# Kernel tuning notes

Measured on AMD Instinct MI355X. Metric: run time of the kernel, lower is better.

## Reference

```python
import jax, jax.numpy as jnp
import numpy as np

DIM = 512
NUM_HEADS = 16
HEAD_DIM = DIM // NUM_HEADS
HIDDEN = int(DIM * 4.0)
EPS = 1e-5


def layer_norm(x, gamma, beta):
    mu = jnp.mean(x, axis=-1, keepdims=True)
    var = jnp.mean(jnp.square(x - mu), axis=-1, keepdims=True)
    return (x - mu) * jax.lax.rsqrt(var + EPS) * gamma + beta


def setup_inputs() -> dict:
    key = jax.random.key(0)
    ks = jax.random.split(key, 8)
    B, L, C = 32, 3136, DIM
    x = jax.random.normal(ks[0], (B, L, C), dtype=jnp.float32)
    norm1_g = jnp.ones((C,), jnp.float32)
    norm1_b = jnp.zeros((C,), jnp.float32)
    # spatial (per-head) mixing weight: (num_heads, head_dim, head_dim)
    w_spatial = jax.random.normal(ks[1], (NUM_HEADS, HEAD_DIM, HEAD_DIM), jnp.float32) * (1.0 / np.sqrt(HEAD_DIM))
    norm2_g = jnp.ones((C,), jnp.float32)
    norm2_b = jnp.zeros((C,), jnp.float32)
    w1 = jax.random.normal(ks[2], (C, HIDDEN), jnp.float32) * (1.0 / np.sqrt(C))
    b1 = jnp.zeros((HIDDEN,), jnp.float32)
    w2 = jax.random.normal(ks[3], (HIDDEN, C), jnp.float32) * (1.0 / np.sqrt(HIDDEN))
    b2 = jnp.zeros((C,), jnp.float32)
    return {"x": x, "norm1_g": norm1_g, "norm1_b": norm1_b, "w_spatial": w_spatial,
            "norm2_g": norm2_g, "norm2_b": norm2_b, "w1": w1, "b1": b1, "w2": w2, "b2": b2}


def reference(x, norm1_g, norm1_b, w_spatial, norm2_g, norm2_b, w1, b1, w2, b2):
    B, L, C = x.shape
    shortcut = x
    h = layer_norm(x, norm1_g, norm1_b)
    # window partition -> per-head channel-sub-dim linear (shared across windows/positions)
    # mathematically equivalent to applying the per-head matmul at every token
    h = h.reshape(B, L, NUM_HEADS, HEAD_DIM)
    h = jnp.einsum('blhd,hde->blhe', h, w_spatial)
    h = h.reshape(B, L, C)
    x = shortcut + h
    # channel MLP: Linear -> GELU(tanh) -> Linear
    y = layer_norm(x, norm2_g, norm2_b)
    y = jax.nn.gelu(y @ w1 + b1, approximate=True)
    y = y @ w2 + b2
    return x + y
```

## Files before the change

### kernel.cpp

```cpp
#include <hip/hip_runtime.h>
#include <hip/hip_bf16.h>


typedef __bf16 bf16x8 __attribute__((ext_vector_type(8)));
typedef float f32x4 __attribute__((ext_vector_type(4)));

constexpr int CDIM = 512;
constexpr int HID = 2048;
constexpr int MROWS = 32 * 3136;
constexpr float LN_EPS = 1e-5f;

static __device__ __forceinline__ float gelu_tanh(float x) {
  const float u = 0.7978845608028654f * fmaf(0.044715f * x * x, x, x);
  const float e = __expf(2.0f * u);
  return 0.5f * x * (2.0f - 2.0f / (e + 1.0f));
}

static __device__ __forceinline__ void load_lds16(const void* g, void* l) {
  __builtin_amdgcn_global_load_lds((__attribute__((address_space(1))) void*)g,
                                   (__attribute__((address_space(3))) void*)l,
                                   16, 0, 0);
}

template <int KD>
__global__ __launch_bounds__(256) void cvt_t(const float* __restrict__ src,
                                             __hip_bfloat16* __restrict__ dst,
                                             int ND) {
  const int i = blockIdx.x * 256 + threadIdx.x;
  const int n = i / KD;
  const int k = i - n * KD;
  dst[i] = __float2bfloat16(src[(size_t)k * ND + n]);
}

__global__ __launch_bounds__(256) void fused_pre(
    const float* __restrict__ x, const float* __restrict__ g1,
    const float* __restrict__ b1, const float* __restrict__ wsp,
    const float* __restrict__ g2, const float* __restrict__ b2,
    float* __restrict__ x2out, __hip_bfloat16* __restrict__ yout) {
  __shared__ float lnbuf[CDIM];
  __shared__ float red[8];

  const int t = threadIdx.x;
  const int lane = t & 63;
  const int w = t >> 6;
  const int c0 = t, c1 = t + 256;
  const int hd0 = c0 >> 5, e0 = c0 & 31;
  const int hd1 = c1 >> 5, e1 = c1 & 31;

  float wc0[32], wc1[32];
#pragma unroll
  for (int d = 0; d < 32; ++d) {
    wc0[d] = wsp[(hd0 * 32 + d) * 32 + e0];
    wc1[d] = wsp[(hd1 * 32 + d) * 32 + e1];
  }
  const float g1v0 = g1[c0], g1v1 = g1[c1], b1v0 = b1[c0], b1v1 = b1[c1];
  const float g2v0 = g2[c0], g2v1 = g2[c1], b2v0 = b2[c0], b2v1 = b2[c1];

  for (int r = blockIdx.x; r < MROWS; r += gridDim.x) {
    const float* xr = x + (size_t)r * CDIM;
    const float xv0 = xr[c0], xv1 = xr[c1];

    float s = xv0 + xv1, ss = xv0 * xv0 + xv1 * xv1;
#pragma unroll
    for (int off = 32; off; off >>= 1) {
      s += __shfl_down(s, off);
      ss += __shfl_down(ss, off);
    }
    if (lane == 0) { red[w * 2] = s; red[w * 2 + 1] = ss; }
    __syncthreads();
    s = red[0] + red[2] + red[4] + red[6];
    ss = red[1] + red[3] + red[5] + red[7];
    float mu = s * (1.0f / CDIM);
    float var = ss * (1.0f / CDIM) - mu * mu;
    float rs = rsqrtf(var + LN_EPS);
    lnbuf[c0] = (xv0 - mu) * rs * g1v0 + b1v0;
    lnbuf[c1] = (xv1 - mu) * rs * g1v1 + b1v1;
    __syncthreads();

    float h0 = 0.f, h1 = 0.f;
#pragma unroll
    for (int d = 0; d < 32; ++d) {
      h0 = fmaf(lnbuf[hd0 * 32 + d], wc0[d], h0);
      h1 = fmaf(lnbuf[hd1 * 32 + d], wc1[d], h1);
    }
    const float a0 = xv0 + h0, a1 = xv1 + h1;
    x2out[(size_t)r * CDIM + c0] = a0;
    x2out[(size_t)r * CDIM + c1] = a1;

    s = a0 + a1;
    ss = a0 * a0 + a1 * a1;
#pragma unroll
    for (int off = 32; off; off >>= 1) {
      s += __shfl_down(s, off);
      ss += __shfl_down(ss, off);
    }
    if (lane == 0) { red[w * 2] = s; red[w * 2 + 1] = ss; }
    __syncthreads();
    s = red[0] + red[2] + red[4] + red[6];
    ss = red[1] + red[3] + red[5] + red[7];
    mu = s * (1.0f / CDIM);
    var = ss * (1.0f / CDIM) - mu * mu;
    rs = rsqrtf(var + LN_EPS);
    yout[(size_t)r * CDIM + c0] = __float2bfloat16((a0 - mu) * rs * g2v0 + b2v0);
    yout[(size_t)r * CDIM + c1] = __float2bfloat16((a1 - mu) * rs * g2v1 + b2v1);
    __syncthreads();
  }
}

template <int K, int N, bool GELU>
__global__ __launch_bounds__(512, 2) void gemm8p(
    const __hip_bfloat16* __restrict__ A, const __hip_bfloat16* __restrict__ Bt,
    const float* __restrict__ bias, __hip_bfloat16* __restrict__ zout,
    float* __restrict__ fout) {
  constexpr int NT = N / 256;
  constexpr int NKT = K / 32;
  __shared__ __attribute__((aligned(16))) __hip_bfloat16 lds[4][2][256 * 32];

  const int tid = threadIdx.x;
  const int lane = tid & 63;
  const int w = tid >> 6;
  const int wm = w >> 2, wn = w & 3;

  const int cpx = gridDim.x >> 3;
  const int bid = (blockIdx.x & 7) * cpx + (blockIdx.x >> 3);
  const int tm = bid / NT, tn = bid - tm * NT;
  const size_t am0 = (size_t)tm * 256;
  const int bn0 = tn * 256;

  const int r0 = tid >> 2;
  const int ks0 = (tid & 3) ^ ((tid >> 2) & 3) ^ ((tid >> 4) & 3);
  const __hip_bfloat16* aP0 = A + (am0 + r0) * K + ks0 * 8;
  const __hip_bfloat16* aP1 = aP0 + (size_t)128 * K;
  const __hip_bfloat16* bP0 = Bt + (size_t)(bn0 + r0) * K + ks0 * 8;
  const __hip_bfloat16* bP1 = bP0 + (size_t)128 * K;
  const int lo0 = (w * 64) * 8;
  const int lo1 = (512 + w * 64) * 8;

#define STAGE_A(sl, kt)                            \
  do {                                             \
    load_lds16(aP0 + (kt) * 32, &lds[sl][0][lo0]); \
    load_lds16(aP1 + (kt) * 32, &lds[sl][0][lo1]); \
  } while (0)
#define STAGE_B(sl, kt)                            \
  do {                                             \
    load_lds16(bP0 + (kt) * 32, &lds[sl][1][lo0]); \
    load_lds16(bP1 + (kt) * 32, &lds[sl][1][lo1]); \
  } while (0)

  f32x4 acc[8][4] = {};
  const int fr = lane & 15;
  const int kgs = (((lane >> 4) ^ (lane & 3) ^ ((lane >> 2) & 3))) * 8;

  STAGE_A(0, 0);
  STAGE_B(0, 0);
  STAGE_A(1, 1);
  STAGE_B(1, 1);

  for (int t = 0; t < NKT; ++t) {
    if (t + 1 < NKT)
      asm volatile("s_waitcnt vmcnt(4)" ::: "memory");
    else
      asm volatile("s_waitcnt vmcnt(0)" ::: "memory");
    __builtin_amdgcn_s_barrier();

    const int sl = t & 3;
    const int s2 = (t + 2) & 3;
    const bool pf = (t + 2) < NKT;
    const __hip_bfloat16* As = lds[sl][0];
    const __hip_bfloat16* Bs = lds[sl][1];

    if (pf) STAGE_A(s2, t + 2);
    bf16x8 bfv[4];
#pragma unroll
    for (int n = 0; n < 4; ++n)
      bfv[n] = *(const bf16x8*)(Bs + (wn * 64 + n * 16 + fr) * 32 + kgs);
    bf16x8 af[4];
#pragma unroll
    for (int m = 0; m < 4; ++m)
      af[m] = *(const bf16x8*)(As + (wm * 128 + m * 16 + fr) * 32 + kgs);
    __builtin_amdgcn_s_setprio(1);
#pragma unroll
    for (int m = 0; m < 4; ++m)
#pragma unroll
      for (int n = 0; n < 4; ++n)
        acc[m][n] = __builtin_amdgcn_mfma_f32_16x16x32_bf16(af[m], bfv[n],
                                                            acc[m][n], 0, 0, 0);
    __builtin_amdgcn_s_setprio(0);
    __builtin_amdgcn_s_barrier();

    if (pf) STAGE_B(s2, t + 2);
#pragma unroll
    for (int m = 0; m < 4; ++m)
      af[m] = *(const bf16x8*)(As + (wm * 128 + (m + 4) * 16 + fr) * 32 + kgs);
    __builtin_amdgcn_s_setprio(1);
#pragma unroll
    for (int m = 0; m < 4; ++m)
#pragma unroll
      for (int n = 0; n < 4; ++n)
        acc[m + 4][n] = __builtin_amdgcn_mfma_f32_16x16x32_bf16(
            af[m], bfv[n], acc[m + 4][n], 0, 0, 0);
    __builtin_amdgcn_s_setprio(0);
  }
#undef STAGE_A
#undef STAGE_B

  const int cr = (lane >> 4) * 4;
  const int cc = lane & 15;
#pragma unroll
  for (int n = 0; n < 4; ++n) {
    const int col = bn0 + wn * 64 + n * 16 + cc;
    const float bv = bias[col];
#pragma unroll
    for (int m = 0; m < 8; ++m) {
      const size_t row = am0 + wm * 128 + m * 16 + cr;
#pragma unroll
      for (int j = 0; j < 4; ++j) {
        const float v = acc[m][n][j] + bv;
        const size_t off = (row + j) * N + col;
        if constexpr (GELU) {
          zout[off] = __float2bfloat16(gelu_tanh(v));
        } else {
          fout[off] = fout[off] + v;
        }
      }
    }
  }
}

extern "C" void kernel_launch(void* const* d_in, const int* in_sizes, int n_in,
                              void* d_out, int out_size, void* d_ws,
                              size_t ws_size, hipStream_t stream) {
  const float* x = (const float*)d_in[0];
  const float* n1g = (const float*)d_in[1];
  const float* n1b = (const float*)d_in[2];
  const float* wsp = (const float*)d_in[3];
  const float* n2g = (const float*)d_in[4];
  const float* n2b = (const float*)d_in[5];
  const float* w1 = (const float*)d_in[6];
  const float* b1 = (const float*)d_in[7];
  const float* w2 = (const float*)d_in[8];
  const float* b2 = (const float*)d_in[9];
  float* out = (float*)d_out;

  __hip_bfloat16* ybuf = (__hip_bfloat16*)d_ws;
  __hip_bfloat16* zbuf = ybuf + (size_t)MROWS * CDIM;
  __hip_bfloat16* w1t = zbuf + (size_t)MROWS * HID;
  __hip_bfloat16* w2t = w1t + (size_t)CDIM * HID;

  cvt_t<CDIM><<<(CDIM * HID) / 256, 256, 0, stream>>>(w1, w1t, HID);
  cvt_t<HID><<<(CDIM * HID) / 256, 256, 0, stream>>>(w2, w2t, CDIM);
  fused_pre<<<2048, 256, 0, stream>>>(x, n1g, n1b, wsp, n2g, n2b, out, ybuf);
  gemm8p<CDIM, HID, true><<<(MROWS / 256) * (HID / 256), 512, 0, stream>>>(
      ybuf, w1t, b1, zbuf, nullptr);
  gemm8p<HID, CDIM, false><<<(MROWS / 256) * (CDIM / 256), 512, 0, stream>>>(
      zbuf, w2t, b2, nullptr, out);
}
```

Before: 939.3 us.

## Stage GEMM epilogues through LDS for coalesced stores; vectorize transpose and LN

The GEMM epilogues now write the accumulator tile into shared memory and then emit 16-byte coalesced global stores. For the second GEMM this also applies to the read-modify-write residual add, done in two row halves to fit LDS. The weight transpose kernel uses a padded LDS tile with float4 reads, and the LayerNorm kernel moves to float2 loads and stores per thread. This targets the scattered 2- and 4-byte epilogue stores, at the cost of extra barriers and LDS traffic after the main loop.

```diff
diff --git a/kernel.cpp b/kernel.cpp
--- a/kernel.cpp
+++ b/kernel.cpp
@@ -22,14 +22,34 @@
                                    16, 0, 0);
 }
 
-template <int KD>
+template <int KD, int ND>
 __global__ __launch_bounds__(256) void cvt_t(const float* __restrict__ src,
-                                             __hip_bfloat16* __restrict__ dst,
-                                             int ND) {
-  const int i = blockIdx.x * 256 + threadIdx.x;
-  const int n = i / KD;
-  const int k = i - n * KD;
-  dst[i] = __float2bfloat16(src[(size_t)k * ND + n]);
+                                             __hip_bfloat16* __restrict__ dst) {
+  __shared__ float tl[64][65];
+  const int t = threadIdx.x;
+  constexpr int NTN = ND / 64;
+  const int k0 = (blockIdx.x / NTN) * 64;
+  const int n0 = (blockIdx.x % NTN) * 64;
+  const int c4 = (t & 15) * 4;
+  const int r = t >> 4;
+#pragma unroll
+  for (int j = 0; j < 4; ++j) {
+    const int kk = r + j * 16;
+    const float4 v = *(const float4*)&src[(size_t)(k0 + kk) * ND + n0 + c4];
+    tl[c4 + 0][kk] = v.x;
+    tl[c4 + 1][kk] = v.y;
+    tl[c4 + 2][kk] = v.z;
+    tl[c4 + 3][kk] = v.w;
+  }
+  __syncthreads();
+#pragma unroll
+  for (int j = 0; j < 4; ++j) {
+    const int nn = r + j * 16;
+    __hip_bfloat16 o[4];
+#pragma unroll
+    for (int c = 0; c < 4; ++c) o[c] = __float2bfloat16(tl[nn][c4 + c]);
+    *(uint2*)&dst[(size_t)(n0 + nn) * KD + k0 + c4] = *(const uint2*)o;
+  }
 }
 
 __global__ __launch_bounds__(256) void fused_pre(
@@ -43,24 +63,25 @@
   const int t = threadIdx.x;
   const int lane = t & 63;
   const int w = t >> 6;
-  const int c0 = t, c1 = t + 256;
-  const int hd0 = c0 >> 5, e0 = c0 & 31;
-  const int hd1 = c1 >> 5, e1 = c1 & 31;
+  const int c0 = 2 * t;
+  const int hd = c0 >> 5, e0 = c0 & 31;
 
   float wc0[32], wc1[32];
 #pragma unroll
   for (int d = 0; d < 32; ++d) {
-    wc0[d] = wsp[(hd0 * 32 + d) * 32 + e0];
-    wc1[d] = wsp[(hd1 * 32 + d) * 32 + e1];
-  }
-  const float g1v0 = g1[c0], g1v1 = g1[c1], b1v0 = b1[c0], b1v1 = b1[c1];
-  const float g2v0 = g2[c0], g2v1 = g2[c1], b2v0 = b2[c0], b2v1 = b2[c1];
+    const float2 wv = *(const float2*)&wsp[(hd * 32 + d) * 32 + e0];
+    wc0[d] = wv.x;
+    wc1[d] = wv.y;
+  }
+  const float2 g1v = *(const float2*)&g1[c0];
+  const float2 b1v = *(const float2*)&b1[c0];
+  const float2 g2v = *(const float2*)&g2[c0];
+  const float2 b2v = *(const float2*)&b2[c0];
 
   for (int r = blockIdx.x; r < MROWS; r += gridDim.x) {
-    const float* xr = x + (size_t)r * CDIM;
-    const float xv0 = xr[c0], xv1 = xr[c1];
-
-    float s = xv0 + xv1, ss = xv0 * xv0 + xv1 * xv1;
+    const float2 xv = *(const float2*)&x[(size_t)r * CDIM + c0];
+
+    float s = xv.x + xv.y, ss = xv.x * xv.x + xv.y * xv.y;
 #pragma unroll
     for (int off = 32; off; off >>= 1) {
       s += __shfl_down(s, off);
@@ -73,19 +94,22 @@
     float mu = s * (1.0f / CDIM);
     float var = ss * (1.0f / CDIM) - mu * mu;
     float rs = rsqrtf(var + LN_EPS);
-    lnbuf[c0] = (xv0 - mu) * rs * g1v0 + b1v0;
-    lnbuf[c1] = (xv1 - mu) * rs * g1v1 + b1v1;
+    lnbuf[c0] = (xv.x - mu) * rs * g1v.x + b1v.x;
+    lnbuf[c0 + 1] = (xv.y - mu) * rs * g1v.y + b1v.y;
     __syncthreads();
 
     float h0 = 0.f, h1 = 0.f;
 #pragma unroll
     for (int d = 0; d < 32; ++d) {
-      h0 = fmaf(lnbuf[hd0 * 32 + d], wc0[d], h0);
-      h1 = fmaf(lnbuf[hd1 * 32 + d], wc1[d], h1);
-    }
-    const float a0 = xv0 + h0, a1 = xv1 + h1;
-    x2out[(size_t)r * CDIM + c0] = a0;
-    x2out[(size_t)r * CDIM + c1] = a1;
+      const float lv = lnbuf[hd * 32 + d];
+      h0 = fmaf(lv, wc0[d], h0);
+      h1 = fmaf(lv, wc1[d], h1);
+    }
+    const float a0 = xv.x + h0, a1 = xv.y + h1;
+    float2 av;
+    av.x = a0;
+    av.y = a1;
+    *(float2*)&x2out[(size_t)r * CDIM + c0] = av;
 
     s = a0 + a1;
     ss = a0 * a0 + a1 * a1;
@@ -101,8 +125,10 @@
     mu = s * (1.0f / CDIM);
     var = ss * (1.0f / CDIM) - mu * mu;
     rs = rsqrtf(var + LN_EPS);
-    yout[(size_t)r * CDIM + c0] = __float2bfloat16((a0 - mu) * rs * g2v0 + b2v0);
-    yout[(size_t)r * CDIM + c1] = __float2bfloat16((a1 - mu) * rs * g2v1 + b2v1);
+    __hip_bfloat162 yv;
+    yv.x = __float2bfloat16((a0 - mu) * rs * g2v.x + b2v.x);
+    yv.y = __float2bfloat16((a1 - mu) * rs * g2v.y + b2v.y);
+    *(__hip_bfloat162*)&yout[(size_t)r * CDIM + c0] = yv;
     __syncthreads();
   }
 }
@@ -206,22 +232,64 @@
 
   const int cr = (lane >> 4) * 4;
   const int cc = lane & 15;
-#pragma unroll
-  for (int n = 0; n < 4; ++n) {
-    const int col = bn0 + wn * 64 + n * 16 + cc;
-    const float bv = bias[col];
-#pragma unroll
-    for (int m = 0; m < 8; ++m) {
-      const size_t row = am0 + wm * 128 + m * 16 + cr;
-#pragma unroll
-      for (int j = 0; j < 4; ++j) {
-        const float v = acc[m][n][j] + bv;
-        const size_t off = (row + j) * N + col;
-        if constexpr (GELU) {
-          zout[off] = __float2bfloat16(gelu_tanh(v));
-        } else {
-          fout[off] = fout[off] + v;
+  char* smb = (char*)&lds[0][0][0];
+
+  if constexpr (GELU) {
+    __syncthreads();
+    __hip_bfloat16* ot = (__hip_bfloat16*)smb;
+#pragma unroll
+    for (int n = 0; n < 4; ++n) {
+      const int col = wn * 64 + n * 16 + cc;
+      const float bv = bias[bn0 + col];
+#pragma unroll
+      for (int m = 0; m < 8; ++m) {
+        const int row = wm * 128 + m * 16 + cr;
+#pragma unroll
+        for (int j = 0; j < 4; ++j)
+          ot[(row + j) * 256 + col] =
+              __float2bfloat16(gelu_tanh(acc[m][n][j] + bv));
+      }
+    }
+    __syncthreads();
+#pragma unroll
+    for (int it = 0; it < 16; ++it) {
+      const int seg = it * 512 + tid;
+      const int row = seg >> 5, cs = seg & 31;
+      const uint4 v = *(const uint4*)(smb + seg * 16);
+      *(uint4*)&zout[(am0 + row) * N + bn0 + cs * 8] = v;
+    }
+  } else {
+    float* ot = (float*)smb;
+#pragma unroll
+    for (int p = 0; p < 2; ++p) {
+      __syncthreads();
+      if (wm == p) {
+#pragma unroll
+        for (int n = 0; n < 4; ++n) {
+          const int col = wn * 64 + n * 16 + cc;
+          const float bv = bias[bn0 + col];
+#pragma unroll
+          for (int m = 0; m < 8; ++m) {
+            const int rl = m * 16 + cr;
+#pragma unroll
+            for (int j = 0; j < 4; ++j)
+              ot[(rl + j) * 256 + col] = acc[m][n][j] + bv;
+          }
         }
+      }
+      __syncthreads();
+#pragma unroll
+      for (int it = 0; it < 16; ++it) {
+        const int seg = it * 512 + tid;
+        const int row = seg >> 6, cs = seg & 63;
+        const float4 lv = *(const float4*)(smb + seg * 16);
+        float* gp = &fout[(am0 + p * 128 + row) * N + bn0 + cs * 4];
+        float4 o = *(const float4*)gp;
+        o.x += lv.x;
+        o.y += lv.y;
+        o.z += lv.z;
+        o.w += lv.w;
+        *(float4*)gp = o;
       }
     }
   }
@@ -247,8 +315,8 @@
   __hip_bfloat16* w1t = zbuf + (size_t)MROWS * HID;
   __hip_bfloat16* w2t = w1t + (size_t)CDIM * HID;
 
-  cvt_t<CDIM><<<(CDIM * HID) / 256, 256, 0, stream>>>(w1, w1t, HID);
-  cvt_t<HID><<<(CDIM * HID) / 256, 256, 0, stream>>>(w2, w2t, CDIM);
+  cvt_t<CDIM, HID><<<(CDIM / 64) * (HID / 64), 256, 0, stream>>>(w1, w1t);
+  cvt_t<HID, CDIM><<<(HID / 64) * (CDIM / 64), 256, 0, stream>>>(w2, w2t);
   fused_pre<<<2048, 256, 0, stream>>>(x, n1g, n1b, wsp, n2g, n2b, out, ybuf);
   gemm8p<CDIM, HID, true><<<(MROWS / 256) * (HID / 256), 512, 0, stream>>>(
       ybuf, w1t, b1, zbuf, nullptr);
```

Result: no change. 938.0 us (-0.1%).
